# Kernel tuning notes

Hardware: AMD Instinct MI355X
Metric: run time of the kernel (lower is better)

## Reference

```python
import jax, jax.numpy as jnp
import numpy as np

H, N2, R = 512, 16, 32   # hidden_dim, state_dim//2, dt_rank=ceil(512/16)
B, L = 1, 4096


def setup_inputs() -> dict:
    key = jax.random.key(0)
    ks = jax.random.split(key, 7)
    u = jax.random.normal(ks[0], (B, L, H), dtype=jnp.float32)
    # Parameter initialization mirroring S4DKernel.__init__
    A_log = jnp.zeros((H, N2), jnp.float32)                      # log(ones)
    A_im = jnp.broadcast_to(jnp.arange(N2, dtype=jnp.float32), (H, N2)).copy()
    B_param = jax.random.normal(ks[1], (H, N2, 2), jnp.float32)
    C_param = jax.random.normal(ks[2], (H, N2, 2), jnp.float32)
    D = jax.random.normal(ks[3], (H,), jnp.float32)
    dt_w = jax.random.normal(ks[4], (H, R), jnp.float32) / np.sqrt(R)
    dt_min, dt_max, dt_floor = 1e-3, 0.1, 1e-4
    dt_init = jnp.exp(jax.random.uniform(ks[5], (H,), jnp.float32)
                      * (np.log(dt_max) - np.log(dt_floor)) + np.log(dt_floor))
    dt_init = jnp.maximum(dt_init, dt_min)
    dt_b = dt_init + jnp.log(-jnp.expm1(-dt_init))               # inverse-softplus init
    xproj_w = jax.random.normal(ks[6], (R, H), jnp.float32) / np.sqrt(H)
    return {"u": u, "A_log": A_log, "A_im": A_im, "B_param": B_param,
            "C_param": C_param, "D": D, "dt_w": dt_w, "dt_b": dt_b,
            "xproj_w": xproj_w}


def reference(u, A_log, A_im, B_param, C_param, D, dt_w, dt_b, xproj_w):
    # Complex continuous-time parameters
    A = -jnp.exp(A_log) + 1j * A_im                 # [H, N2]
    Bc = B_param[..., 0] + 1j * B_param[..., 1]     # [H, N2]
    Cc = C_param[..., 0] + 1j * C_param[..., 1]     # [H, N2]

    # dt path: x_proj_for_dt (no bias) -> dt_proj -> softplus
    dt_u = jnp.einsum('blh,rh->blr', u, xproj_w)                    # [B,L,R]
    dt = jax.nn.softplus(jnp.einsum('blr,hr->blh', dt_u, dt_w) + dt_b)  # [B,L,H]

    # ZOH discretization
    z = dt[..., None] * A                           # [B,L,H,N2] complex
    A_bar = jnp.exp(z)
    B_bar_div = jnp.where(jnp.abs(z) < 1e-4, 1.0 + z / 2, (jnp.exp(z) - 1.0) / z)
    ub = u[..., None].astype(A_bar.dtype) * B_bar_div * Bc          # [B,L,H,N2]

    # Parallel scan for h_k = A_k * h_{k-1} + u_k (first-order linear recurrence)
    def op(c1, c2):
        a1, b1 = c1
        a2, b2 = c2
        return a1 * a2, a2 * b1 + b2
    _, h = jax.lax.associative_scan(op, (A_bar, ub), axis=1)        # [B,L,H,N2]

    y = jnp.einsum('blhn,hn->blh', h, Cc) + u * D
    return y.real
```

## Files before the change

kernel.cpp:

```cpp
#include <hip/hip_runtime.h>

#define Hd 512
#define N2d 16
#define Rd 32
#define Ld 4096
#define NCHUNK 128
#define CLEN (Ld / NCHUNK)
#define NCH (Hd * N2d)
#define NGRP 16
#define NGROUPS (NCHUNK / NGRP)

__device__ __forceinline__ bool load_consts4(const float* A_log, const float* A_im,
        const float* B_param, int hnb,
        float* Are, float* Aim, float* BAr, float* BAi) {
    #pragma unroll
    for (int j = 0; j < 4; ++j) {
        int hn = hnb + j;
        Are[j] = -__expf(A_log[hn]);
        Aim[j] = A_im[hn];
        float Bre = B_param[2 * hn];
        float Bim = B_param[2 * hn + 1];
        float inv = __builtin_amdgcn_rcpf(Are[j] * Are[j] + Aim[j] * Aim[j]);
        BAr[j] = (Bre * Are[j] + Bim * Aim[j]) * inv;
        BAi[j] = (Bim * Are[j] - Bre * Aim[j]) * inv;
    }
    float d1 = Aim[1] - Aim[0], d2 = Aim[2] - Aim[1], d3 = Aim[3] - Aim[2];
    return (Are[1] == Are[0]) && (Are[2] == Are[0]) && (Are[3] == Are[0]) &&
           (d1 == d2) && (d2 == d3);
}

__global__ __launch_bounds__(256) void k_dt(const float* __restrict__ u,
                                            const float* __restrict__ xproj_w,
                                            const float* __restrict__ dt_w,
                                            const float* __restrict__ dt_b,
                                            float2* __restrict__ du_out) {
    __shared__ float u_s[8][Hd];
    __shared__ float dtu_s[8][Rd];
    const int t = threadIdx.x;
    const int l0 = blockIdx.x * 8;

    #pragma unroll
    for (int i = 0; i < 16; ++i) {
        int idx = t + i * 256;
        ((float*)u_s)[idx] = u[l0 * Hd + idx];
    }
    __syncthreads();

    const int r = t >> 3;
    const int j = t & 7;
    float part[8];
    #pragma unroll
    for (int l = 0; l < 8; ++l) part[l] = 0.f;
    for (int k = 0; k < 64; ++k) {
        float w = xproj_w[r * Hd + k * 8 + j];
        #pragma unroll
        for (int l = 0; l < 8; ++l) part[l] = fmaf(u_s[l][k * 8 + j], w, part[l]);
    }
    #pragma unroll
    for (int off = 1; off < 8; off <<= 1) {
        #pragma unroll
        for (int l = 0; l < 8; ++l) part[l] += __shfl_xor(part[l], off);
    }
    if (j == 0) {
        #pragma unroll
        for (int l = 0; l < 8; ++l) dtu_s[l][r] = part[l];
    }
    __syncthreads();

    #pragma unroll
    for (int hb = 0; hb < 2; ++hb) {
        int h = hb * 256 + t;
        float bias = dt_b[h];
        float acc[8];
        #pragma unroll
        for (int l = 0; l < 8; ++l) acc[l] = bias;
        #pragma unroll
        for (int rb = 0; rb < 8; ++rb) {
            float4 w = *(const float4*)&dt_w[h * Rd + rb * 4];
            #pragma unroll
            for (int l = 0; l < 8; ++l) {
                acc[l] = fmaf(dtu_s[l][rb * 4 + 0], w.x, acc[l]);
                acc[l] = fmaf(dtu_s[l][rb * 4 + 1], w.y, acc[l]);
                acc[l] = fmaf(dtu_s[l][rb * 4 + 2], w.z, acc[l]);
                acc[l] = fmaf(dtu_s[l][rb * 4 + 3], w.w, acc[l]);
            }
        }
        #pragma unroll
        for (int l = 0; l < 8; ++l) {
            float x = acc[l];
            float sp = fmaxf(x, 0.f) + log1pf(__expf(-fabsf(x)));
            float uv = u_s[l][h];
            float us = uv * __builtin_amdgcn_rcpf(fmaxf(sp, 1e-30f));
            du_out[(l0 + l) * Hd + h] = make_float2(sp, us);
        }
    }
}

__global__ __launch_bounds__(256) void k_chunk(const float2* __restrict__ du,
        const float* __restrict__ A_log, const float* __restrict__ A_im,
        const float* __restrict__ B_param, const float* __restrict__ C_param,
        const float* __restrict__ Dp,
        float4* __restrict__ PS, float2* __restrict__ y1T) {
    const int t = threadIdx.x;
    const int q = t & 3;
    const int hh = blockIdx.y * 64 + (t >> 2);
    const int c = blockIdx.x;
    const int hnb = hh * N2d + q * 4;
    const int lbase = c * CLEN;

    float Are[4], Aim[4], BAr[4], BAi[4], Cre[4], Cim[4];
    const bool fast = load_consts4(A_log, A_im, B_param, hnb, Are, Aim, BAr, BAi);
    #pragma unroll
    for (int jj = 0; jj < 4; ++jj) {
        Cre[jj] = C_param[2 * (hnb + jj)];
        Cim[jj] = C_param[2 * (hnb + jj) + 1];
    }
    const float Dv = Dp[hh];

    float sr[4] = {0.f, 0.f, 0.f, 0.f}, si[4] = {0.f, 0.f, 0.f, 0.f};
    float sdt = 0.f;

    float2 b0[8], b1[8];

    #define LOADB(buf, bb)                                                     \
        { _Pragma("unroll")                                                    \
          for (int k = 0; k < 8; ++k)                                          \
              buf[k] = du[(lbase + (bb) * 8 + k) * Hd + hh]; }

    if (fast) {
        const float Are0 = Are[0], Aim0 = Aim[0], dA = Aim[1] - Aim[0];
        #define STEPF(buf, bb)                                                 \
            { _Pragma("unroll")                                                \
              for (int k = 0; k < 8; ++k) {                                    \
                int l = lbase + (bb) * 8 + k;                                  \
                float dtv = buf[k].x, us = buf[k].y;                           \
                sdt += dtv;                                                    \
                float er = __expf(dtv * Are0);                                 \
                float s0, c0, sd, cd;                                          \
                __sincosf(dtv * Aim0, &s0, &c0);                               \
                __sincosf(dtv * dA, &sd, &cd);                                 \
                float ar = er * c0, ai = er * s0;                              \
                float yv = 0.f;                                                \
                _Pragma("unroll")                                              \
                for (int jj = 0; jj < 4; ++jj) {                               \
                    float gr = fmaf(ar, us, -us);                              \
                    float gi = ai * us;                                        \
                    float nr = fmaf(ar, sr[jj], fmaf(-ai, si[jj],              \
                                 fmaf(gr, BAr[jj], -gi * BAi[jj])));           \
                    float ni = fmaf(ar, si[jj], fmaf( ai, sr[jj],              \
                                 fmaf(gr, BAi[jj],  gi * BAr[jj])));           \
                    sr[jj] = nr; si[jj] = ni;                                  \
                    yv = fmaf(nr, Cre[jj], fmaf(-ni, Cim[jj], yv));            \
                    if (jj < 3) {                                              \
                        float tr = fmaf(ar, cd, -ai * sd);                     \
                        ai = fmaf(ai, cd, ar * sd);                            \
                        ar = tr;                                               \
                    }                                                          \
                }                                                              \
                yv += __shfl_xor(yv, 1);                                       \
                yv += __shfl_xor(yv, 2);                                       \
                if (q == 0)                                                    \
                    y1T[l * Hd + hh] = make_float2(fmaf(dtv * us, Dv, yv), sdt);\
              } }
        LOADB(b0, 0);
        LOADB(b1, 1); STEPF(b0, 0);
        LOADB(b0, 2); STEPF(b1, 1);
        LOADB(b1, 3); STEPF(b0, 2);
        STEPF(b1, 3);
        #undef STEPF
    } else {
        #define STEPS(buf, bb)                                                 \
            { _Pragma("unroll")                                                \
              for (int k = 0; k < 8; ++k) {                                    \
                int l = lbase + (bb) * 8 + k;                                  \
                float dtv = buf[k].x, us = buf[k].y;                           \
                sdt += dtv;                                                    \
                float yv = 0.f;                                                \
                _Pragma("unroll")                                              \
                for (int jj = 0; jj < 4; ++jj) {                               \
                    float er = __expf(dtv * Are[jj]);                          \
                    float s, cc;                                               \
                    __sincosf(dtv * Aim[jj], &s, &cc);                         \
                    float ar = er * cc, ai = er * s;                           \
                    float gr = fmaf(ar, us, -us);                              \
                    float gi = ai * us;                                        \
                    float nr = fmaf(ar, sr[jj], fmaf(-ai, si[jj],              \
                                 fmaf(gr, BAr[jj], -gi * BAi[jj])));           \
                    float ni = fmaf(ar, si[jj], fmaf( ai, sr[jj],              \
                                 fmaf(gr, BAi[jj],  gi * BAr[jj])));           \
                    sr[jj] = nr; si[jj] = ni;                                  \
                    yv = fmaf(nr, Cre[jj], fmaf(-ni, Cim[jj], yv));            \
                }                                                              \
                yv += __shfl_xor(yv, 1);                                       \
                yv += __shfl_xor(yv, 2);                                       \
                if (q == 0)                                                    \
                    y1T[l * Hd + hh] = make_float2(fmaf(dtv * us, Dv, yv), sdt);\
              } }
        LOADB(b0, 0);
        LOADB(b1, 1); STEPS(b0, 0);
        LOADB(b0, 2); STEPS(b1, 1);
        LOADB(b1, 3); STEPS(b0, 2);
        STEPS(b1, 3);
        #undef STEPS
    }
    #undef LOADB

    int base = c * NCH + hnb;
    #pragma unroll
    for (int jj = 0; jj < 4; ++jj) {
        float er = __expf(sdt * Are[jj]);
        float s, cc;
        __sincosf(sdt * Aim[jj], &s, &cc);
        PS[base + jj] = make_float4(er * cc, er * s, sr[jj], si[jj]);
    }
}

__global__ __launch_bounds__(256) void k_comb(const float4* __restrict__ PS,
                                              const float* __restrict__ C_param,
                                              float2* __restrict__ W) {
    __shared__ float4 agg_s[32][NGROUPS + 1];
    const int t = threadIdx.x;
    const int g = t >> 5;
    const int cl = t & 31;
    const int chain = blockIdx.x * 32 + cl;

    float4 ps[NGRP];
    #pragma unroll
    for (int i = 0; i < NGRP; ++i)
        ps[i] = PS[(g * NGRP + i) * NCH + chain];

    float pr = 1.f, pi = 0.f, hr = 0.f, hi = 0.f;
    #pragma unroll
    for (int i = 0; i < NGRP; ++i) {
        float nhr = fmaf(ps[i].x, hr, fmaf(-ps[i].y, hi, ps[i].z));
        float nhi = fmaf(ps[i].x, hi, fmaf( ps[i].y, hr, ps[i].w));
        float npr = fmaf(ps[i].x, pr, -ps[i].y * pi);
        float npi = fmaf(ps[i].x, pi,  ps[i].y * pr);
        hr = nhr; hi = nhi; pr = npr; pi = npi;
    }
    agg_s[cl][g] = make_float4(pr, pi, hr, hi);
    __syncthreads();

    float Hr = 0.f, Hi = 0.f;
    for (int j = 0; j < g; ++j) {
        float4 a = agg_s[cl][j];
        float nr = fmaf(a.x, Hr, fmaf(-a.y, Hi, a.z));
        float ni = fmaf(a.x, Hi, fmaf( a.y, Hr, a.w));
        Hr = nr; Hi = ni;
    }

    const float Cr = C_param[2 * chain];
    const float Ci = C_param[2 * chain + 1];
    #pragma unroll
    for (int i = 0; i < NGRP; ++i) {
        int c = g * NGRP + i;
        W[c * NCH + chain] = make_float2(fmaf(Cr, Hr, -Ci * Hi),
                                         fmaf(Cr, Hi,  Ci * Hr));
        float nr = fmaf(ps[i].x, Hr, fmaf(-ps[i].y, Hi, ps[i].z));
        float ni = fmaf(ps[i].x, Hi, fmaf( ps[i].y, Hr, ps[i].w));
        Hr = nr; Hi = ni;
    }
}

__global__ __launch_bounds__(256) void k_corr(const float2* __restrict__ y1T,
        const float* __restrict__ A_log, const float* __restrict__ A_im,
        const float2* __restrict__ W, float* __restrict__ out) {
    const int t = threadIdx.x;
    const int c = blockIdx.x;
    const int hl = t & 63;
    const int h = blockIdx.y * 64 + hl;
    const int lb = t >> 6;
    const int l0 = c * CLEN + lb * 8;
    const int hn0 = h * N2d;

    float2 yt[8];
    #pragma unroll
    for (int k = 0; k < 8; ++k) yt[k] = y1T[(l0 + k) * Hd + h];

    float2 w[N2d];
    #pragma unroll
    for (int n = 0; n < N2d; ++n) w[n] = W[c * NCH + hn0 + n];

    float are[N2d], aim[N2d];
    #pragma unroll
    for (int n = 0; n < N2d; ++n) {
        are[n] = -__expf(A_log[hn0 + n]);
        aim[n] = A_im[hn0 + n];
    }
    float dA = aim[1] - aim[0];
    bool fast = true;
    #pragma unroll
    for (int n = 1; n < N2d; ++n)
        fast = fast && (are[n] == are[0]) && (aim[n] - aim[n - 1] == dA);

    if (fast) {
        const float Are0 = are[0], Aim0 = aim[0];
        #pragma unroll
        for (int k = 0; k < 8; ++k) {
            float T = yt[k].y;
            float er = __expf(Are0 * T);
            float s0, c0, sd, cd;
            __sincosf(Aim0 * T, &s0, &c0);
            __sincosf(dA * T, &sd, &cd);
            float ar = er * c0, ai = er * s0;
            float corr = 0.f;
            #pragma unroll
            for (int n = 0; n < N2d; ++n) {
                corr = fmaf(ar, w[n].x, fmaf(-ai, w[n].y, corr));
                if (n < N2d - 1) {
                    float tr = fmaf(ar, cd, -ai * sd);
                    ai = fmaf(ai, cd, ar * sd);
                    ar = tr;
                }
            }
            out[(l0 + k) * Hd + h] = yt[k].x + corr;
        }
    } else {
        #pragma unroll
        for (int k = 0; k < 8; ++k) {
            float T = yt[k].y;
            float corr = 0.f;
            #pragma unroll
            for (int n = 0; n < N2d; ++n) {
                float er = __expf(are[n] * T);
                float s, cc;
                __sincosf(aim[n] * T, &s, &cc);
                corr = fmaf(er * cc, w[n].x, fmaf(-er * s, w[n].y, corr));
            }
            out[(l0 + k) * Hd + h] = yt[k].x + corr;
        }
    }
}

extern "C" void kernel_launch(void* const* d_in, const int* in_sizes, int n_in,
                              void* d_out, int out_size, void* d_ws, size_t ws_size,
                              hipStream_t stream) {
    const float* u        = (const float*)d_in[0];
    const float* A_log    = (const float*)d_in[1];
    const float* A_im     = (const float*)d_in[2];
    const float* B_param  = (const float*)d_in[3];
    const float* C_param  = (const float*)d_in[4];
    const float* Dp       = (const float*)d_in[5];
    const float* dt_w     = (const float*)d_in[6];
    const float* dt_b     = (const float*)d_in[7];
    const float* xproj_w  = (const float*)d_in[8];

    float2* du  = (float2*)d_ws;
    float4* PS  = (float4*)(du + (size_t)Ld * Hd);
    float2* W   = (float2*)(PS + (size_t)NCHUNK * NCH);
    float2* y1T = W + (size_t)NCHUNK * NCH;
    float*  out = (float*)d_out;

    k_dt<<<Ld / 8, 256, 0, stream>>>(u, xproj_w, dt_w, dt_b, du);
    dim3 g2(NCHUNK, Hd / 64);
    k_chunk<<<g2, 256, 0, stream>>>(du, A_log, A_im, B_param, C_param, Dp, PS, y1T);
    k_comb<<<NCH / 32, 256, 0, stream>>>(PS, C_param, W);
    k_corr<<<g2, 256, 0, stream>>>(y1T, A_log, A_im, W, out);
}
```

Measured before the change: 134.3 us.

## Double chunk count and recompute chunk decay in combine kernel

Doubles the number of scan chunks so each chunk covers 16 timesteps, giving more parallel blocks in the chunk and correction kernels. The chunk kernel no longer computes and stores the per-channel chunk decay as a float4. It stores only the end state plus one accumulated dt per head, and the combine kernel recomputes exp and sincos from that dt. The combine kernel is reorganized to one block per head, which lets it cache the chunk dt values in shared memory, and it writes a table of -exp(A_log) that the correction kernel reuses. The cost is more chunks to combine serially and more transcendental work in the combine step.

```diff
diff --git a/kernel.cpp b/kernel.cpp
--- a/kernel.cpp
+++ b/kernel.cpp
@@ -4,7 +4,7 @@
 #define N2d 16
 #define Rd 32
 #define Ld 4096
-#define NCHUNK 128
+#define NCHUNK 256
 #define CLEN (Ld / NCHUNK)
 #define NCH (Hd * N2d)
 #define NGRP 16
@@ -100,7 +100,8 @@
         const float* __restrict__ A_log, const float* __restrict__ A_im,
         const float* __restrict__ B_param, const float* __restrict__ C_param,
         const float* __restrict__ Dp,
-        float4* __restrict__ PS, float2* __restrict__ y1T) {
+        float2* __restrict__ Sb, float* __restrict__ Tc,
+        float2* __restrict__ y1T) {
     const int t = threadIdx.x;
     const int q = t & 3;
     const int hh = blockIdx.y * 64 + (t >> 2);
@@ -120,19 +121,19 @@
     float sr[4] = {0.f, 0.f, 0.f, 0.f}, si[4] = {0.f, 0.f, 0.f, 0.f};
     float sdt = 0.f;
 
-    float2 b0[8], b1[8];
+    float2 b0[4], b1[4];
 
     #define LOADB(buf, bb)                                                     \
         { _Pragma("unroll")                                                    \
-          for (int k = 0; k < 8; ++k)                                          \
-              buf[k] = du[(lbase + (bb) * 8 + k) * Hd + hh]; }
+          for (int k = 0; k < 4; ++k)                                          \
+              buf[k] = du[(lbase + (bb) * 4 + k) * Hd + hh]; }
 
     if (fast) {
         const float Are0 = Are[0], Aim0 = Aim[0], dA = Aim[1] - Aim[0];
         #define STEPF(buf, bb)                                                 \
             { _Pragma("unroll")                                                \
-              for (int k = 0; k < 8; ++k) {                                    \
-                int l = lbase + (bb) * 8 + k;                                  \
+              for (int k = 0; k < 4; ++k) {                                    \
+                int l = lbase + (bb) * 4 + k;                                  \
                 float dtv = buf[k].x, us = buf[k].y;                           \
                 sdt += dtv;                                                    \
                 float er = __expf(dtv * Are0);                                 \
@@ -171,8 +172,8 @@
     } else {
         #define STEPS(buf, bb)                                                 \
             { _Pragma("unroll")                                                \
-              for (int k = 0; k < 8; ++k) {                                    \
-                int l = lbase + (bb) * 8 + k;                                  \
+              for (int k = 0; k < 4; ++k) {                                    \
+                int l = lbase + (bb) * 4 + k;                                  \
                 float dtv = buf[k].x, us = buf[k].y;                           \
                 sdt += dtv;                                                    \
                 float yv = 0.f;                                                \
@@ -207,46 +208,62 @@
 
     int base = c * NCH + hnb;
     #pragma unroll
-    for (int jj = 0; jj < 4; ++jj) {
-        float er = __expf(sdt * Are[jj]);
-        float s, cc;
-        __sincosf(sdt * Aim[jj], &s, &cc);
-        PS[base + jj] = make_float4(er * cc, er * s, sr[jj], si[jj]);
-    }
-}
-
-__global__ __launch_bounds__(256) void k_comb(const float4* __restrict__ PS,
-                                              const float* __restrict__ C_param,
-                                              float2* __restrict__ W) {
-    __shared__ float4 agg_s[32][NGROUPS + 1];
+    for (int jj = 0; jj < 4; ++jj)
+        Sb[base + jj] = make_float2(sr[jj], si[jj]);
+    if (q == 0) Tc[c * Hd + hh] = sdt;
+}
+
+__global__ __launch_bounds__(256) void k_comb(const float2* __restrict__ Sb,
+        const float* __restrict__ Tc, const float* __restrict__ A_log,
+        const float* __restrict__ A_im, const float* __restrict__ C_param,
+        float2* __restrict__ W, float* __restrict__ Aretab) {
+    __shared__ float4 agg_s[16][NGROUPS + 1];
+    __shared__ float Tc_s[NCHUNK];
     const int t = threadIdx.x;
-    const int g = t >> 5;
-    const int cl = t & 31;
-    const int chain = blockIdx.x * 32 + cl;
-
-    float4 ps[NGRP];
-    #pragma unroll
-    for (int i = 0; i < NGRP; ++i)
-        ps[i] = PS[(g * NGRP + i) * NCH + chain];
-
-    float pr = 1.f, pi = 0.f, hr = 0.f, hi = 0.f;
+    const int g = t >> 4;
+    const int cl = t & 15;
+    const int h = blockIdx.x;
+    const int chain = h * N2d + cl;
+
+    Tc_s[t] = Tc[t * Hd + h];
+    __syncthreads();
+
+    const float Are = -__expf(A_log[chain]);
+    const float Aim = A_im[chain];
+    if (g == 0) Aretab[chain] = Are;
+
+    float pr[NGRP], pi[NGRP];
+    float2 s[NGRP];
     #pragma unroll
     for (int i = 0; i < NGRP; ++i) {
-        float nhr = fmaf(ps[i].x, hr, fmaf(-ps[i].y, hi, ps[i].z));
-        float nhi = fmaf(ps[i].x, hi, fmaf( ps[i].y, hr, ps[i].w));
-        float npr = fmaf(ps[i].x, pr, -ps[i].y * pi);
-        float npi = fmaf(ps[i].x, pi,  ps[i].y * pr);
-        hr = nhr; hi = nhi; pr = npr; pi = npi;
-    }
-    agg_s[cl][g] = make_float4(pr, pi, hr, hi);
+        int c = g * NGRP + i;
+        s[i] = Sb[c * NCH + chain];
+        float T = Tc_s[c];
+        float er = __expf(Are * T);
+        float sn, cs;
+        __sincosf(Aim * T, &sn, &cs);
+        pr[i] = er * cs;
+        pi[i] = er * sn;
+    }
+
+    float Pr = 1.f, Pi = 0.f, Hr = 0.f, Hi = 0.f;
+    #pragma unroll
+    for (int i = 0; i < NGRP; ++i) {
+        float nhr = fmaf(pr[i], Hr, fmaf(-pi[i], Hi, s[i].x));
+        float nhi = fmaf(pr[i], Hi, fmaf( pi[i], Hr, s[i].y));
+        float npr = fmaf(pr[i], Pr, -pi[i] * Pi);
+        float npi = fmaf(pr[i], Pi,  pi[i] * Pr);
+        Hr = nhr; Hi = nhi; Pr = npr; Pi = npi;
+    }
+    agg_s[cl][g] = make_float4(Pr, Pi, Hr, Hi);
     __syncthreads();
 
-    float Hr = 0.f, Hi = 0.f;
+    float hr = 0.f, hi = 0.f;
     for (int j = 0; j < g; ++j) {
         float4 a = agg_s[cl][j];
-        float nr = fmaf(a.x, Hr, fmaf(-a.y, Hi, a.z));
-        float ni = fmaf(a.x, Hi, fmaf( a.y, Hr, a.w));
-        Hr = nr; Hi = ni;
+        float nr = fmaf(a.x, hr, fmaf(-a.y, hi, a.z));
+        float ni = fmaf(a.x, hi, fmaf( a.y, hr, a.w));
+        hr = nr; hi = ni;
     }
 
     const float Cr = C_param[2 * chain];
@@ -254,28 +271,28 @@
     #pragma unroll
     for (int i = 0; i < NGRP; ++i) {
         int c = g * NGRP + i;
-        W[c * NCH + chain] = make_float2(fmaf(Cr, Hr, -Ci * Hi),
-                                         fmaf(Cr, Hi,  Ci * Hr));
-        float nr = fmaf(ps[i].x, Hr, fmaf(-ps[i].y, Hi, ps[i].z));
-        float ni = fmaf(ps[i].x, Hi, fmaf( ps[i].y, Hr, ps[i].w));
-        Hr = nr; Hi = ni;
+        W[c * NCH + chain] = make_float2(fmaf(Cr, hr, -Ci * hi),
+                                         fmaf(Cr, hi,  Ci * hr));
+        float nr = fmaf(pr[i], hr, fmaf(-pi[i], hi, s[i].x));
+        float ni = fmaf(pr[i], hi, fmaf( pi[i], hr, s[i].y));
+        hr = nr; hi = ni;
     }
 }
 
 __global__ __launch_bounds__(256) void k_corr(const float2* __restrict__ y1T,
-        const float* __restrict__ A_log, const float* __restrict__ A_im,
+        const float* __restrict__ Aretab, const float* __restrict__ A_im,
         const float2* __restrict__ W, float* __restrict__ out) {
     const int t = threadIdx.x;
     const int c = blockIdx.x;
     const int hl = t & 63;
     const int h = blockIdx.y * 64 + hl;
     const int lb = t >> 6;
-    const int l0 = c * CLEN + lb * 8;
+    const int l0 = c * CLEN + lb * 4;
     const int hn0 = h * N2d;
 
-    float2 yt[8];
-    #pragma unroll
-    for (int k = 0; k < 8; ++k) yt[k] = y1T[(l0 + k) * Hd + h];
+    float2 yt[4];
+    #pragma unroll
+    for (int k = 0; k < 4; ++k) yt[k] = y1T[(l0 + k) * Hd + h];
 
     float2 w[N2d];
     #pragma unroll
@@ -284,7 +301,7 @@
     float are[N2d], aim[N2d];
     #pragma unroll
     for (int n = 0; n < N2d; ++n) {
-        are[n] = -__expf(A_log[hn0 + n]);
+        are[n] = Aretab[hn0 + n];
         aim[n] = A_im[hn0 + n];
     }
     float dA = aim[1] - aim[0];
@@ -296,7 +313,7 @@
     if (fast) {
         const float Are0 = are[0], Aim0 = aim[0];
         #pragma unroll
-        for (int k = 0; k < 8; ++k) {
+        for (int k = 0; k < 4; ++k) {
             float T = yt[k].y;
             float er = __expf(Are0 * T);
             float s0, c0, sd, cd;
@@ -317,7 +334,7 @@
         }
     } else {
         #pragma unroll
-        for (int k = 0; k < 8; ++k) {
+        for (int k = 0; k < 4; ++k) {
             float T = yt[k].y;
             float corr = 0.f;
             #pragma unroll
@@ -345,15 +362,18 @@
     const float* dt_b     = (const float*)d_in[7];
     const float* xproj_w  = (const float*)d_in[8];
 
-    float2* du  = (float2*)d_ws;
-    float4* PS  = (float4*)(du + (size_t)Ld * Hd);
-    float2* W   = (float2*)(PS + (size_t)NCHUNK * NCH);
-    float2* y1T = W + (size_t)NCHUNK * NCH;
-    float*  out = (float*)d_out;
+    float2* du     = (float2*)d_ws;
+    float2* Sb     = du + (size_t)Ld * Hd;
+    float2* W      = Sb + (size_t)NCHUNK * NCH;
+    float2* y1T    = W + (size_t)NCHUNK * NCH;
+    float*  Tc     = (float*)(y1T + (size_t)Ld * Hd);
+    float*  Aretab = Tc + (size_t)NCHUNK * Hd;
+    float*  out    = (float*)d_out;
 
     k_dt<<<Ld / 8, 256, 0, stream>>>(u, xproj_w, dt_w, dt_b, du);
     dim3 g2(NCHUNK, Hd / 64);
-    k_chunk<<<g2, 256, 0, stream>>>(du, A_log, A_im, B_param, C_param, Dp, PS, y1T);
-    k_comb<<<NCH / 32, 256, 0, stream>>>(PS, C_param, W);
-    k_corr<<<g2, 256, 0, stream>>>(y1T, A_log, A_im, W, out);
-}
+    k_chunk<<<g2, 256, 0, stream>>>(du, A_log, A_im, B_param, C_param, Dp,
+                                    Sb, Tc, y1T);
+    k_comb<<<Hd, 256, 0, stream>>>(Sb, Tc, A_log, A_im, C_param, W, Aretab);
+    k_corr<<<g2, 256, 0, stream>>>(y1T, Aretab, A_im, W, out);
+}
```

After: 140.8 us. 4.9% more time.
